# Optimization experiments

Hardware: AMD Instinct MI355X
Metric: run time of the kernel (lower is better)

## Reference

```python
import jax, jax.numpy as jnp
import numpy as np

NUM_NODES = 80000
NUM_EDGES = 1280000
NUM_GRAPHS = 512
IN_DIM = 64
HID = 64
NUM_CLASSES = 10


def setup_inputs() -> dict:
    key = jax.random.key(0)
    ks = jax.random.split(key, 16)
    x = jax.random.normal(ks[0], (NUM_NODES, IN_DIM), dtype=jnp.float32)
    edge_index = jax.random.randint(ks[1], (2, NUM_EDGES), 0, NUM_NODES, dtype=jnp.int64)
    batch = jnp.sort(jax.random.randint(ks[2], (NUM_NODES,), 0, NUM_GRAPHS, dtype=jnp.int64))

    def glorot(k, shape):
        fan_in, fan_out = shape[1], shape[0]
        lim = jnp.sqrt(6.0 / (fan_in + fan_out))
        return jax.random.uniform(k, shape, dtype=jnp.float32, minval=-lim, maxval=lim)

    inp = {
        "x": x,
        "edge_index": edge_index,
        "batch": batch,
        # GraphConv layer 1: lin_rel (with bias) applied to aggregated neighbors, lin_root (no bias)
        "w_rel1": glorot(ks[3], (HID, IN_DIM)),
        "b_rel1": jnp.zeros((HID,), dtype=jnp.float32),
        "w_root1": glorot(ks[4], (HID, IN_DIM)),
        # layer 2
        "w_rel2": glorot(ks[5], (HID, HID)),
        "b_rel2": jnp.zeros((HID,), dtype=jnp.float32),
        "w_root2": glorot(ks[6], (HID, HID)),
        # layer 3
        "w_rel3": glorot(ks[7], (HID, HID)),
        "b_rel3": jnp.zeros((HID,), dtype=jnp.float32),
        "w_root3": glorot(ks[8], (HID, HID)),
        # final linear head
        "w_lin": glorot(ks[9], (NUM_CLASSES, HID)),
        "b_lin": jnp.zeros((NUM_CLASSES,), dtype=jnp.float32),
    }
    return inp


def _graph_conv(x, src, dst, w_rel, b_rel, w_root):
    # PyG GraphConv with aggr='add': out_i = W_rel @ (sum_{j in N(i)} x_j) + b_rel + W_root @ x_i
    agg = jax.ops.segment_sum(x[src], dst, num_segments=NUM_NODES)  # [N, d_in]
    return agg @ w_rel.T + b_rel + x @ w_root.T


def reference(x, edge_index, batch,
              w_rel1, b_rel1, w_root1,
              w_rel2, b_rel2, w_root2,
              w_rel3, b_rel3, w_root3,
              w_lin, b_lin):
    src, dst = edge_index[0], edge_index[1]
    h = jax.nn.relu(_graph_conv(x, src, dst, w_rel1, b_rel1, w_root1))
    h = jax.nn.relu(_graph_conv(h, src, dst, w_rel2, b_rel2, w_root2))
    h = _graph_conv(h, src, dst, w_rel3, b_rel3, w_root3)
    # global_mean_pool over graph ids
    sums = jax.ops.segment_sum(h, batch, num_segments=NUM_GRAPHS)          # [G, HID]
    counts = jax.ops.segment_sum(jnp.ones((h.shape[0],), h.dtype), batch, num_segments=NUM_GRAPHS)
    pooled = sums / jnp.maximum(counts, 1.0)[:, None]
    # dropout p=0.5 is identity at inference (training=False)
    return pooled @ w_lin.T + b_lin  # [G, NUM_CLASSES]
```

## Files before the change

kernel.cpp:

```cpp
#include <hip/hip_runtime.h>

#define N_NODES  80000
#define N_EDGES  1280000
#define N_GRAPHS 512
#define DIM      64
#define NCLS     10

#define ETILE    8192
#define NTILE    157
#define NCB      157
#define CBPAD    160

typedef short short8f __attribute__((ext_vector_type(8)));
typedef float float4f __attribute__((ext_vector_type(4)));

static __device__ __forceinline__ unsigned short f2bf(float f) {
    unsigned u = __float_as_uint(f);
    unsigned r = (u + 0x7FFFu + ((u >> 16) & 1u)) >> 16;
    return (unsigned short)r;
}
static __device__ __forceinline__ float bf_lo(unsigned v) { return __uint_as_float(v << 16); }
static __device__ __forceinline__ float bf_hi(unsigned v) { return __uint_as_float(v & 0xFFFF0000u); }

__global__ __launch_bounds__(256) void k_histprep(const int* __restrict__ ei,
        const float* __restrict__ x,
        const float* __restrict__ wr1, const float* __restrict__ wo1,
        const float* __restrict__ wr2, const float* __restrict__ wo2,
        int* __restrict__ hmat, unsigned short* __restrict__ xb,
        unsigned short* __restrict__ wf) {
    __shared__ int hist[NCB];
    int bid = blockIdx.x, t = threadIdx.x;
    if (bid < NTILE) {
        int tile = bid;
        for (int i = t; i < NCB; i += 256) hist[i] = 0;
        __syncthreads();
        int base = tile * ETILE;
        int end = base + ETILE; if (end > N_EDGES) end = N_EDGES;
        for (int i = base + t; i < end; i += 256)
            atomicAdd(&hist[ei[N_EDGES + i] >> 9], 1);
        __syncthreads();
        for (int i = t; i < NCB; i += 256) hmat[tile * CBPAD + i] = hist[i];
        return;
    }
    int pb = bid - NTILE;
    if (pb < 5000) {
        int i = pb * 256 + t;
        float4 v = ((const float4*)x)[i];
        ushort4 o;
        o.x = f2bf(v.x); o.y = f2bf(v.y); o.z = f2bf(v.z); o.w = f2bf(v.w);
        ((ushort4*)xb)[i] = o;
    } else {
        int idx = (pb - 5000) * 256 + t;
        int j = idx & 7, lane = (idx >> 3) & 63;
        int ks = (idx >> 9) & 3, nt = (idx >> 11) & 3, l = idx >> 13;
        int k = ks * 32 + ((lane >> 4) & 3) * 8 + j;
        int n = nt * 16 + (lane & 15);
        const float* wr = (l == 0) ? wr1 : wr2;
        const float* wo = (l == 0) ? wo1 : wo2;
        float val = (k < 64) ? wr[n * 64 + k] : wo[n * 64 + (k - 64)];
        wf[idx] = f2bf(val);
    }
}

__global__ __launch_bounds__(256) void k_scanT(const int* __restrict__ hmat,
        int* __restrict__ obase, int* __restrict__ btot) {
    __shared__ int sa[256], sb[256];
    int b = blockIdx.x, t = threadIdx.x;
    int v = (t < NTILE) ? hmat[t * CBPAD + b] : 0;
    sa[t] = v; __syncthreads();
    int* sp = sa; int* dp = sb;
    for (int off = 1; off < 256; off <<= 1) {
        dp[t] = sp[t] + ((t >= off) ? sp[t - off] : 0);
        __syncthreads();
        int* tmp = sp; sp = dp; dp = tmp;
    }
    int incl = sp[t];
    if (t < NTILE) obase[t * CBPAD + b] = incl - v;
    if (t == NTILE - 1) btot[b] = incl;
}

__global__ __launch_bounds__(256) void k_scatter2(const int* __restrict__ ei,
        const int* __restrict__ obase, const int* __restrict__ btot,
        int* __restrict__ ebuf) {
    __shared__ int sa[256], sb[256];
    __shared__ int cur[NCB];
    int tile = blockIdx.x, t = threadIdx.x;
    int v = (t < NCB) ? btot[t] : 0;
    sa[t] = v; __syncthreads();
    int* sp = sa; int* dp = sb;
    for (int off = 1; off < 256; off <<= 1) {
        dp[t] = sp[t] + ((t >= off) ? sp[t - off] : 0);
        __syncthreads();
        int* tmp = sp; sp = dp; dp = tmp;
    }
    if (t < NCB) cur[t] = (sp[t] - v) + obase[tile * CBPAD + t];
    __syncthreads();
    int base = tile * ETILE;
    int end = base + ETILE; if (end > N_EDGES) end = N_EDGES;
    for (int i = base + t; i < end; i += 256) {
        int s = ei[i], d = ei[N_EDGES + i];
        int p = atomicAdd(&cur[d >> 9], 1);
        ebuf[p] = s | ((d & 511) << 17);
    }
}

__global__ __launch_bounds__(256) void k_csr2(const int* __restrict__ ebuf,
        const int* __restrict__ btot, int* __restrict__ rowptr,
        int* __restrict__ col) {
    __shared__ int cnt[512];
    __shared__ int sa[512], sb[512];
    __shared__ int cur[512];
    int b = blockIdx.x, t = threadIdx.x;
    int v = (t < NCB) ? btot[t] : 0;
    sa[t] = v; __syncthreads();
    int* sp = sa; int* dp = sb;
    for (int off = 1; off < 256; off <<= 1) {
        dp[t] = sp[t] + ((t >= off) ? sp[t - off] : 0);
        __syncthreads();
        int* tmp = sp; sp = dp; dp = tmp;
    }
    int e = sp[b];
    int s = e - btot[b];
    if (b == 0 && t == 0) rowptr[N_NODES] = N_EDGES;
    __syncthreads();
    cnt[t] = 0; cnt[t + 256] = 0;
    __syncthreads();
    for (int i = s + t; i < e; i += 256) atomicAdd(&cnt[ebuf[i] >> 17], 1);
    __syncthreads();
    sa[t] = cnt[t]; sa[t + 256] = cnt[t + 256];
    __syncthreads();
    sp = sa; dp = sb;
    for (int off = 1; off < 512; off <<= 1) {
        int i1 = t + 256;
        int v0 = sp[t]  + ((t  >= off) ? sp[t  - off] : 0);
        int v1 = sp[i1] + ((i1 >= off) ? sp[i1 - off] : 0);
        __syncthreads();
        dp[t] = v0; dp[i1] = v1;
        __syncthreads();
        int* tmp = sp; sp = dp; dp = tmp;
    }
    int node0 = b * 512;
    int base0 = s + sp[t] - cnt[t];
    int base1 = s + sp[t + 256] - cnt[t + 256];
    cur[t] = base0; cur[t + 256] = base1;
    if (node0 + t < N_NODES)       rowptr[node0 + t] = base0;
    if (node0 + t + 256 < N_NODES) rowptr[node0 + t + 256] = base1;
    __syncthreads();
    for (int i = s + t; i < e; i += 256) {
        int pk = ebuf[i];
        int p = atomicAdd(&cur[pk >> 17], 1);
        col[p] = pk & 0x1FFFF;
    }
}

__global__ __launch_bounds__(256) void k_gatherlin(
        const unsigned short* __restrict__ Xin,
        const int* __restrict__ rowptr, const int* __restrict__ col,
        const unsigned short* __restrict__ wf, const float* __restrict__ bias,
        unsigned short* __restrict__ out, int relu) {
    __shared__ uint4 sAgg[64][9];
    const uint4* Xq = (const uint4*)Xin;
    int t = threadIdx.x, w = t >> 6, lane = t & 63;
    int e = lane >> 3, c = lane & 7;
    int nb = blockIdx.x * 64 + w * 16;
    int rp = (lane <= 16) ? rowptr[nb + lane] : 0;
    for (int n = 0; n < 16; ++n) {
        int start = __shfl(rp, n), end = __shfl(rp, n + 1);
        float acc[8] = {0.f, 0.f, 0.f, 0.f, 0.f, 0.f, 0.f, 0.f};
        int base = start;
        for (; base + 16 <= end; base += 16) {
            int i0 = col[base + e];
            int i1 = col[base + 8 + e];
            uint4 v0 = Xq[(size_t)i0 * 8 + c];
            uint4 v1 = Xq[(size_t)i1 * 8 + c];
            acc[0] += bf_lo(v0.x) + bf_lo(v1.x); acc[1] += bf_hi(v0.x) + bf_hi(v1.x);
            acc[2] += bf_lo(v0.y) + bf_lo(v1.y); acc[3] += bf_hi(v0.y) + bf_hi(v1.y);
            acc[4] += bf_lo(v0.z) + bf_lo(v1.z); acc[5] += bf_hi(v0.z) + bf_hi(v1.z);
            acc[6] += bf_lo(v0.w) + bf_lo(v1.w); acc[7] += bf_hi(v0.w) + bf_hi(v1.w);
        }
        for (; base + 8 <= end; base += 8) {
            int i0 = col[base + e];
            uint4 v0 = Xq[(size_t)i0 * 8 + c];
            acc[0] += bf_lo(v0.x); acc[1] += bf_hi(v0.x);
            acc[2] += bf_lo(v0.y); acc[3] += bf_hi(v0.y);
            acc[4] += bf_lo(v0.z); acc[5] += bf_hi(v0.z);
            acc[6] += bf_lo(v0.w); acc[7] += bf_hi(v0.w);
        }
        int r = end - base;
        if (e < r) {
            int i0 = col[base + e];
            uint4 v0 = Xq[(size_t)i0 * 8 + c];
            acc[0] += bf_lo(v0.x); acc[1] += bf_hi(v0.x);
            acc[2] += bf_lo(v0.y); acc[3] += bf_hi(v0.y);
            acc[4] += bf_lo(v0.z); acc[5] += bf_hi(v0.z);
            acc[6] += bf_lo(v0.w); acc[7] += bf_hi(v0.w);
        }
#pragma unroll
        for (int off = 8; off < 64; off <<= 1) {
#pragma unroll
            for (int j = 0; j < 8; ++j) acc[j] += __shfl_xor(acc[j], off);
        }
        if (e == 0) {
            uint4 o;
            o.x = (unsigned)f2bf(acc[0]) | ((unsigned)f2bf(acc[1]) << 16);
            o.y = (unsigned)f2bf(acc[2]) | ((unsigned)f2bf(acc[3]) << 16);
            o.z = (unsigned)f2bf(acc[4]) | ((unsigned)f2bf(acc[5]) << 16);
            o.w = (unsigned)f2bf(acc[6]) | ((unsigned)f2bf(acc[7]) << 16);
            sAgg[w * 16 + n][c] = o;
        }
    }
    int quad = lane >> 4, l15 = lane & 15;
    int m = nb + l15;
    short8f a0 = *(const short8f*)&sAgg[w * 16 + l15][quad];
    short8f a1 = *(const short8f*)&sAgg[w * 16 + l15][4 + quad];
    const unsigned short* xr = Xin + (size_t)m * 64;
    short8f a2 = *(const short8f*)(xr + quad * 8);
    short8f a3 = *(const short8f*)(xr + 32 + quad * 8);
    int orow = nb + quad * 4;
#pragma unroll
    for (int nt = 0; nt < 4; ++nt) {
        const unsigned short* wp = wf + ((size_t)(nt * 4) * 64 + lane) * 8;
        short8f b0 = *(const short8f*)(wp);
        short8f b1 = *(const short8f*)(wp + 64 * 8);
        short8f b2 = *(const short8f*)(wp + 128 * 8);
        short8f b3 = *(const short8f*)(wp + 192 * 8);
        float4f acc = {0.f, 0.f, 0.f, 0.f};
        acc = __builtin_amdgcn_mfma_f32_16x16x32_bf16(a0, b0, acc, 0, 0, 0);
        acc = __builtin_amdgcn_mfma_f32_16x16x32_bf16(a1, b1, acc, 0, 0, 0);
        acc = __builtin_amdgcn_mfma_f32_16x16x32_bf16(a2, b2, acc, 0, 0, 0);
        acc = __builtin_amdgcn_mfma_f32_16x16x32_bf16(a3, b3, acc, 0, 0, 0);
        float bi = bias[nt * 16 + l15];
#pragma unroll
        for (int r = 0; r < 4; ++r) {
            float v = acc[r] + bi;
            if (relu) v = fmaxf(v, 0.f);
            out[(size_t)(orow + r) * 64 + nt * 16 + l15] = f2bf(v);
        }
    }
}

static __device__ __forceinline__ int lowerb(const int* a, int n, int key) {
    int lo = 0, hi = n;
    while (lo < hi) { int mid = (lo + hi) >> 1; if (a[mid] < key) lo = mid + 1; else hi = mid; }
    return lo;
}

__global__ __launch_bounds__(256) void k_gsum(const unsigned short* __restrict__ h2,
        const int* __restrict__ rowptr, const int* __restrict__ col,
        const int* __restrict__ batch, float* __restrict__ S4) {
    __shared__ float red1[8][64];
    __shared__ float red2[8][64];
    const unsigned* Xu = (const unsigned*)h2;
    int g = blockIdx.x >> 2, part = blockIdx.x & 3;
    int t = threadIdx.x;
    int hw = t >> 5, c = t & 31;
    int ns = lowerb(batch, N_NODES, g);
    int ne = lowerb(batch, N_NODES, g + 1);
    int a0 = ns + (int)(((long long)(ne - ns) * part) >> 2);
    int a1 = ns + (int)(((long long)(ne - ns) * (part + 1)) >> 2);
    int es = rowptr[a0], ee = rowptr[a1];
    float alo = 0.f, ahi = 0.f;
    int nfull = (ee - es) >> 7;
    int e0 = es + hw * 16;
    for (int b = 0; b < nfull; ++b, e0 += 128) {
        unsigned v[16];
#pragma unroll
        for (int j = 0; j < 16; ++j)
            v[j] = Xu[(size_t)col[e0 + j] * 32 + c];
#pragma unroll
        for (int j = 0; j < 16; ++j) { alo += bf_lo(v[j]); ahi += bf_hi(v[j]); }
    }
    for (int e = es + nfull * 128 + hw; e < ee; e += 8) {
        unsigned v = Xu[(size_t)col[e] * 32 + c];
        alo += bf_lo(v); ahi += bf_hi(v);
    }
    float blo = 0.f, bhi = 0.f;
    for (int i = a0 + hw; i < a1; i += 8) {
        unsigned v = Xu[(size_t)i * 32 + c];
        blo += bf_lo(v); bhi += bf_hi(v);
    }
    red1[hw][2 * c] = alo; red1[hw][2 * c + 1] = ahi;
    red2[hw][2 * c] = blo; red2[hw][2 * c + 1] = bhi;
    __syncthreads();
    if (t < 64) {
        float v = 0.f;
#pragma unroll
        for (int s = 0; s < 8; ++s) v += red1[s][t];
        S4[(size_t)blockIdx.x * 128 + t] = v;
    } else if (t < 128) {
        float v = 0.f;
#pragma unroll
        for (int s = 0; s < 8; ++s) v += red2[s][t - 64];
        S4[(size_t)blockIdx.x * 128 + 64 + (t - 64)] = v;
    }
}

__global__ __launch_bounds__(64) void k_head2(const float* __restrict__ S4,
        const int* __restrict__ batch,
        const float* __restrict__ wr3, const float* __restrict__ wo3,
        const float* __restrict__ b3,
        const float* __restrict__ wlin, const float* __restrict__ blin,
        float* __restrict__ out) {
    __shared__ float s1[64], s2[64], pl[64];
    int g = blockIdx.x, t = threadIdx.x;
    int ns = lowerb(batch, N_NODES, g);
    int ne = lowerb(batch, N_NODES, g + 1);
    float inv = 1.f / (float)((ne > ns) ? (ne - ns) : 1);
    const float* Sg = S4 + (size_t)g * 4 * 128;
    s1[t] = (Sg[t]       + Sg[128 + t]       + Sg[256 + t]       + Sg[384 + t]) * inv;
    s2[t] = (Sg[64 + t]  + Sg[192 + t]       + Sg[320 + t]       + Sg[448 + t]) * inv;
    __syncthreads();
    float acc = b3[t];
    for (int k = 0; k < 64; ++k)
        acc += s1[k] * wr3[t * 64 + k] + s2[k] * wo3[t * 64 + k];
    pl[t] = acc;
    __syncthreads();
    float myout = 0.f;
    for (int cls = 0; cls < NCLS; ++cls) {
        float vv = pl[t] * wlin[cls * 64 + t];
        for (int off = 32; off > 0; off >>= 1) vv += __shfl_xor(vv, off);
        if (t == cls) myout = vv + blin[cls];
    }
    if (t < NCLS) out[g * NCLS + t] = myout;
}

extern "C" void kernel_launch(void* const* d_in, const int* in_sizes, int n_in,
                              void* d_out, int out_size, void* d_ws, size_t ws_size,
                              hipStream_t stream) {
    const float* x     = (const float*)d_in[0];
    const int*   ei    = (const int*)d_in[1];
    const int*   batch = (const int*)d_in[2];
    const float* wr1 = (const float*)d_in[3];
    const float* b1  = (const float*)d_in[4];
    const float* wo1 = (const float*)d_in[5];
    const float* wr2 = (const float*)d_in[6];
    const float* b2  = (const float*)d_in[7];
    const float* wo2 = (const float*)d_in[8];
    const float* wr3 = (const float*)d_in[9];
    const float* b3  = (const float*)d_in[10];
    const float* wo3 = (const float*)d_in[11];
    const float* wlin = (const float*)d_in[12];
    const float* blin = (const float*)d_in[13];
    float* out = (float*)d_out;

    char* p = (char*)d_ws;
    auto alloc = [&](size_t bytes) { char* r = p; p += (bytes + 255) & ~(size_t)255; return r; };
    int*   rowptr  = (int*)alloc((N_NODES + 1) * sizeof(int));
    int*   hmat    = (int*)alloc((size_t)NTILE * CBPAD * sizeof(int));
    int*   obase   = (int*)alloc((size_t)NTILE * CBPAD * sizeof(int));
    int*   btot    = (int*)alloc(CBPAD * sizeof(int));
    int*   ebuf    = (int*)alloc((size_t)N_EDGES * sizeof(int));
    int*   col     = (int*)alloc((size_t)N_EDGES * sizeof(int));
    unsigned short* wf  = (unsigned short*)alloc(2 * 8192 * sizeof(unsigned short));
    unsigned short* xbf = (unsigned short*)alloc((size_t)N_NODES * 64 * 2);
    unsigned short* hA  = (unsigned short*)alloc((size_t)N_NODES * 64 * 2);
    unsigned short* hB  = (unsigned short*)alloc((size_t)N_NODES * 64 * 2);
    float* S4      = (float*)alloc((size_t)N_GRAPHS * 4 * 128 * sizeof(float));

    k_histprep<<<NTILE + 5064, 256, 0, stream>>>(ei, x, wr1, wo1, wr2, wo2,
                                                 hmat, xbf, wf);
    k_scanT   <<<NCB,   256, 0, stream>>>(hmat, obase, btot);
    k_scatter2<<<NTILE, 256, 0, stream>>>(ei, obase, btot, ebuf);
    k_csr2    <<<NCB,   256, 0, stream>>>(ebuf, btot, rowptr, col);

    k_gatherlin<<<N_NODES / 64, 256, 0, stream>>>(xbf, rowptr, col, wf,        b1, hA, 1);
    k_gatherlin<<<N_NODES / 64, 256, 0, stream>>>(hA,  rowptr, col, wf + 8192, b2, hB, 1);

    k_gsum <<<N_GRAPHS * 4, 256, 0, stream>>>(hB, rowptr, col, batch, S4);
    k_head2<<<N_GRAPHS,     64,  0, stream>>>(S4, batch, wr3, wo3, b3, wlin, blin, out);
}
```

Baseline: 261.7 us.

## Switch activations to fp16 with packed half accumulation and finer CSR bucketing

Stores node features and weights as fp16 instead of bf16, so neighbour aggregation accumulates in packed half8 vector adds and the cross-lane reduction shuffles packed halves, removing per-element unpack-to-float arithmetic. The MFMA calls switch to the f16 variant. Separately, the CSR build uses smaller edge tiles (2048) and 256-node destination buckets, giving more blocks for the histogram, scatter and per-bucket sort kernels, with the scans adapted to handle more entries per thread. Accumulating sums in fp16 lowers precision and risks overflow or accuracy loss on high-degree nodes.

New measurement: 238.7 us. -8.8%, faster.

```diff
diff --git a/kernel.cpp b/kernel.cpp
--- a/kernel.cpp
+++ b/kernel.cpp
@@ -6,21 +6,24 @@
 #define DIM      64
 #define NCLS     10
 
-#define ETILE    8192
-#define NTILE    157
-#define NCB      157
-#define CBPAD    160
-
-typedef short short8f __attribute__((ext_vector_type(8)));
+#define ETILE    2048
+#define NTILE    625
+#define NCB      313
+#define CBPAD    320
+
+typedef _Float16 half8f __attribute__((ext_vector_type(8)));
 typedef float float4f __attribute__((ext_vector_type(4)));
 
-static __device__ __forceinline__ unsigned short f2bf(float f) {
-    unsigned u = __float_as_uint(f);
-    unsigned r = (u + 0x7FFFu + ((u >> 16) & 1u)) >> 16;
-    return (unsigned short)r;
-}
-static __device__ __forceinline__ float bf_lo(unsigned v) { return __uint_as_float(v << 16); }
-static __device__ __forceinline__ float bf_hi(unsigned v) { return __uint_as_float(v & 0xFFFF0000u); }
+static __device__ __forceinline__ unsigned short f2h(float f) {
+    _Float16 h = (_Float16)f;
+    return __builtin_bit_cast(unsigned short, h);
+}
+static __device__ __forceinline__ float h_lo(unsigned v) {
+    return (float)__builtin_bit_cast(_Float16, (unsigned short)(v & 0xFFFF));
+}
+static __device__ __forceinline__ float h_hi(unsigned v) {
+    return (float)__builtin_bit_cast(_Float16, (unsigned short)(v >> 16));
+}
 
 __global__ __launch_bounds__(256) void k_histprep(const int* __restrict__ ei,
         const float* __restrict__ x,
@@ -35,9 +38,9 @@
         for (int i = t; i < NCB; i += 256) hist[i] = 0;
         __syncthreads();
         int base = tile * ETILE;
-        int end = base + ETILE; if (end > N_EDGES) end = N_EDGES;
+        int end = base + ETILE;
         for (int i = base + t; i < end; i += 256)
-            atomicAdd(&hist[ei[N_EDGES + i] >> 9], 1);
+            atomicAdd(&hist[ei[N_EDGES + i] >> 8], 1);
         __syncthreads();
         for (int i = t; i < NCB; i += 256) hmat[tile * CBPAD + i] = hist[i];
         return;
@@ -47,7 +50,7 @@
         int i = pb * 256 + t;
         float4 v = ((const float4*)x)[i];
         ushort4 o;
-        o.x = f2bf(v.x); o.y = f2bf(v.y); o.z = f2bf(v.z); o.w = f2bf(v.w);
+        o.x = f2h(v.x); o.y = f2h(v.y); o.z = f2h(v.z); o.w = f2h(v.w);
         ((ushort4*)xb)[i] = o;
     } else {
         int idx = (pb - 5000) * 256 + t;
@@ -58,7 +61,7 @@
         const float* wr = (l == 0) ? wr1 : wr2;
         const float* wo = (l == 0) ? wo1 : wo2;
         float val = (k < 64) ? wr[n * 64 + k] : wo[n * 64 + (k - 64)];
-        wf[idx] = f2bf(val);
+        wf[idx] = f2h(val);
     }
 }
 
@@ -66,85 +69,96 @@
         int* __restrict__ obase, int* __restrict__ btot) {
     __shared__ int sa[256], sb[256];
     int b = blockIdx.x, t = threadIdx.x;
-    int v = (t < NTILE) ? hmat[t * CBPAD + b] : 0;
-    sa[t] = v; __syncthreads();
+    int j0 = 3 * t;
+    int l0 = (j0     < NTILE) ? hmat[(j0    ) * CBPAD + b] : 0;
+    int l1 = (j0 + 1 < NTILE) ? hmat[(j0 + 1) * CBPAD + b] : 0;
+    int l2 = (j0 + 2 < NTILE) ? hmat[(j0 + 2) * CBPAD + b] : 0;
+    int s = l0 + l1 + l2;
+    sa[t] = s; __syncthreads();
     int* sp = sa; int* dp = sb;
     for (int off = 1; off < 256; off <<= 1) {
         dp[t] = sp[t] + ((t >= off) ? sp[t - off] : 0);
         __syncthreads();
         int* tmp = sp; sp = dp; dp = tmp;
     }
-    int incl = sp[t];
-    if (t < NTILE) obase[t * CBPAD + b] = incl - v;
-    if (t == NTILE - 1) btot[b] = incl;
+    int ex = sp[t] - s;
+    if (j0     < NTILE) obase[(j0    ) * CBPAD + b] = ex;
+    if (j0 + 1 < NTILE) obase[(j0 + 1) * CBPAD + b] = ex + l0;
+    if (j0 + 2 < NTILE) obase[(j0 + 2) * CBPAD + b] = ex + l0 + l1;
+    if (t == 255) btot[b] = sp[255];
 }
 
 __global__ __launch_bounds__(256) void k_scatter2(const int* __restrict__ ei,
         const int* __restrict__ obase, const int* __restrict__ btot,
         int* __restrict__ ebuf) {
     __shared__ int sa[256], sb[256];
+    __shared__ int bbase[NCB];
     __shared__ int cur[NCB];
     int tile = blockIdx.x, t = threadIdx.x;
-    int v = (t < NCB) ? btot[t] : 0;
-    sa[t] = v; __syncthreads();
+    int l0 = (2 * t     < NCB) ? btot[2 * t]     : 0;
+    int l1 = (2 * t + 1 < NCB) ? btot[2 * t + 1] : 0;
+    int s = l0 + l1;
+    sa[t] = s; __syncthreads();
     int* sp = sa; int* dp = sb;
     for (int off = 1; off < 256; off <<= 1) {
         dp[t] = sp[t] + ((t >= off) ? sp[t - off] : 0);
         __syncthreads();
         int* tmp = sp; sp = dp; dp = tmp;
     }
-    if (t < NCB) cur[t] = (sp[t] - v) + obase[tile * CBPAD + t];
+    int ex = sp[t] - s;
+    if (2 * t     < NCB) bbase[2 * t]     = ex;
+    if (2 * t + 1 < NCB) bbase[2 * t + 1] = ex + l0;
+    __syncthreads();
+    for (int i = t; i < NCB; i += 256)
+        cur[i] = bbase[i] + obase[tile * CBPAD + i];
     __syncthreads();
     int base = tile * ETILE;
-    int end = base + ETILE; if (end > N_EDGES) end = N_EDGES;
+    int end = base + ETILE;
     for (int i = base + t; i < end; i += 256) {
-        int s = ei[i], d = ei[N_EDGES + i];
-        int p = atomicAdd(&cur[d >> 9], 1);
-        ebuf[p] = s | ((d & 511) << 17);
+        int sv = ei[i], d = ei[N_EDGES + i];
+        int p = atomicAdd(&cur[d >> 8], 1);
+        ebuf[p] = sv | ((d & 255) << 17);
     }
 }
 
 __global__ __launch_bounds__(256) void k_csr2(const int* __restrict__ ebuf,
         const int* __restrict__ btot, int* __restrict__ rowptr,
         int* __restrict__ col) {
-    __shared__ int cnt[512];
-    __shared__ int sa[512], sb[512];
-    __shared__ int cur[512];
+    __shared__ int sa[256], sb[256];
+    __shared__ int bbase[NCB];
+    __shared__ int cnt[256], cur[256];
     int b = blockIdx.x, t = threadIdx.x;
-    int v = (t < NCB) ? btot[t] : 0;
-    sa[t] = v; __syncthreads();
+    int l0 = (2 * t     < NCB) ? btot[2 * t]     : 0;
+    int l1 = (2 * t + 1 < NCB) ? btot[2 * t + 1] : 0;
+    int sm = l0 + l1;
+    sa[t] = sm; __syncthreads();
     int* sp = sa; int* dp = sb;
     for (int off = 1; off < 256; off <<= 1) {
         dp[t] = sp[t] + ((t >= off) ? sp[t - off] : 0);
         __syncthreads();
         int* tmp = sp; sp = dp; dp = tmp;
     }
-    int e = sp[b];
-    int s = e - btot[b];
-    if (b == 0 && t == 0) rowptr[N_NODES] = N_EDGES;
-    __syncthreads();
-    cnt[t] = 0; cnt[t + 256] = 0;
-    __syncthreads();
+    int ex = sp[t] - sm;
+    if (2 * t     < NCB) bbase[2 * t]     = ex;
+    if (2 * t + 1 < NCB) bbase[2 * t + 1] = ex + l0;
+    cnt[t] = 0;
+    __syncthreads();
+    int s = bbase[b];
+    int e = s + btot[b];
     for (int i = s + t; i < e; i += 256) atomicAdd(&cnt[ebuf[i] >> 17], 1);
     __syncthreads();
-    sa[t] = cnt[t]; sa[t + 256] = cnt[t + 256];
-    __syncthreads();
+    int c = cnt[t];
+    sa[t] = c; __syncthreads();
     sp = sa; dp = sb;
-    for (int off = 1; off < 512; off <<= 1) {
-        int i1 = t + 256;
-        int v0 = sp[t]  + ((t  >= off) ? sp[t  - off] : 0);
-        int v1 = sp[i1] + ((i1 >= off) ? sp[i1 - off] : 0);
-        __syncthreads();
-        dp[t] = v0; dp[i1] = v1;
+    for (int off = 1; off < 256; off <<= 1) {
+        dp[t] = sp[t] + ((t >= off) ? sp[t - off] : 0);
         __syncthreads();
         int* tmp = sp; sp = dp; dp = tmp;
     }
-    int node0 = b * 512;
-    int base0 = s + sp[t] - cnt[t];
-    int base1 = s + sp[t + 256] - cnt[t + 256];
-    cur[t] = base0; cur[t + 256] = base1;
-    if (node0 + t < N_NODES)       rowptr[node0 + t] = base0;
-    if (node0 + t + 256 < N_NODES) rowptr[node0 + t + 256] = base1;
+    int rowbase = s + sp[t] - c;
+    cur[t] = rowbase;
+    int node = b * 256 + t;
+    if (node <= N_NODES) rowptr[node] = rowbase;
     __syncthreads();
     for (int i = s + t; i < e; i += 256) {
         int pk = ebuf[i];
@@ -159,82 +173,68 @@
         const unsigned short* __restrict__ wf, const float* __restrict__ bias,
         unsigned short* __restrict__ out, int relu) {
     __shared__ uint4 sAgg[64][9];
-    const uint4* Xq = (const uint4*)Xin;
+    const half8f* Xq = (const half8f*)Xin;
     int t = threadIdx.x, w = t >> 6, lane = t & 63;
     int e = lane >> 3, c = lane & 7;
     int nb = blockIdx.x * 64 + w * 16;
     int rp = (lane <= 16) ? rowptr[nb + lane] : 0;
     for (int n = 0; n < 16; ++n) {
         int start = __shfl(rp, n), end = __shfl(rp, n + 1);
-        float acc[8] = {0.f, 0.f, 0.f, 0.f, 0.f, 0.f, 0.f, 0.f};
+        half8f acc = {};
         int base = start;
         for (; base + 16 <= end; base += 16) {
             int i0 = col[base + e];
             int i1 = col[base + 8 + e];
-            uint4 v0 = Xq[(size_t)i0 * 8 + c];
-            uint4 v1 = Xq[(size_t)i1 * 8 + c];
-            acc[0] += bf_lo(v0.x) + bf_lo(v1.x); acc[1] += bf_hi(v0.x) + bf_hi(v1.x);
-            acc[2] += bf_lo(v0.y) + bf_lo(v1.y); acc[3] += bf_hi(v0.y) + bf_hi(v1.y);
-            acc[4] += bf_lo(v0.z) + bf_lo(v1.z); acc[5] += bf_hi(v0.z) + bf_hi(v1.z);
-            acc[6] += bf_lo(v0.w) + bf_lo(v1.w); acc[7] += bf_hi(v0.w) + bf_hi(v1.w);
+            half8f v0 = Xq[(size_t)i0 * 8 + c];
+            half8f v1 = Xq[(size_t)i1 * 8 + c];
+            acc = acc + v0;
+            acc = acc + v1;
         }
         for (; base + 8 <= end; base += 8) {
             int i0 = col[base + e];
-            uint4 v0 = Xq[(size_t)i0 * 8 + c];
-            acc[0] += bf_lo(v0.x); acc[1] += bf_hi(v0.x);
-            acc[2] += bf_lo(v0.y); acc[3] += bf_hi(v0.y);
-            acc[4] += bf_lo(v0.z); acc[5] += bf_hi(v0.z);
-            acc[6] += bf_lo(v0.w); acc[7] += bf_hi(v0.w);
+            acc = acc + Xq[(size_t)i0 * 8 + c];
         }
         int r = end - base;
         if (e < r) {
             int i0 = col[base + e];
-            uint4 v0 = Xq[(size_t)i0 * 8 + c];
-            acc[0] += bf_lo(v0.x); acc[1] += bf_hi(v0.x);
-            acc[2] += bf_lo(v0.y); acc[3] += bf_hi(v0.y);
-            acc[4] += bf_lo(v0.z); acc[5] += bf_hi(v0.z);
-            acc[6] += bf_lo(v0.w); acc[7] += bf_hi(v0.w);
+            acc = acc + Xq[(size_t)i0 * 8 + c];
         }
 #pragma unroll
         for (int off = 8; off < 64; off <<= 1) {
-#pragma unroll
-            for (int j = 0; j < 8; ++j) acc[j] += __shfl_xor(acc[j], off);
-        }
-        if (e == 0) {
-            uint4 o;
-            o.x = (unsigned)f2bf(acc[0]) | ((unsigned)f2bf(acc[1]) << 16);
-            o.y = (unsigned)f2bf(acc[2]) | ((unsigned)f2bf(acc[3]) << 16);
-            o.z = (unsigned)f2bf(acc[4]) | ((unsigned)f2bf(acc[5]) << 16);
-            o.w = (unsigned)f2bf(acc[6]) | ((unsigned)f2bf(acc[7]) << 16);
-            sAgg[w * 16 + n][c] = o;
-        }
+            uint4 au = __builtin_bit_cast(uint4, acc);
+            uint4 bu;
+            bu.x = __shfl_xor(au.x, off); bu.y = __shfl_xor(au.y, off);
+            bu.z = __shfl_xor(au.z, off); bu.w = __shfl_xor(au.w, off);
+            acc = acc + __builtin_bit_cast(half8f, bu);
+        }
+        if (e == 0) sAgg[w * 16 + n][c] = __builtin_bit_cast(uint4, acc);
     }
     int quad = lane >> 4, l15 = lane & 15;
     int m = nb + l15;
-    short8f a0 = *(const short8f*)&sAgg[w * 16 + l15][quad];
-    short8f a1 = *(const short8f*)&sAgg[w * 16 + l15][4 + quad];
-    const unsigned short* xr = Xin + (size_t)m * 64;
-    short8f a2 = *(const short8f*)(xr + quad * 8);
-    short8f a3 = *(const short8f*)(xr + 32 + quad * 8);
+    half8f a0 = *(const half8f*)&sAgg[w * 16 + l15][quad];
+    half8f a1 = *(const half8f*)&sAgg[w * 16 + l15][4 + quad];
+    const half8f* xr = (const half8f*)(Xin + (size_t)m * 64);
+    half8f a2 = xr[quad];
+    half8f a3 = xr[4 + quad];
     int orow = nb + quad * 4;
 #pragma unroll
     for (int nt = 0; nt < 4; ++nt) {
-        const unsigned short* wp = wf + ((size_t)(nt * 4) * 64 + lane) * 8;
-        short8f b0 = *(const short8f*)(wp);
-        short8f b1 = *(const short8f*)(wp + 64 * 8);
-        short8f b2 = *(const short8f*)(wp + 128 * 8);
-        short8f b3 = *(const short8f*)(wp + 192 * 8);
+        const half8f* wp = (const half8f*)(wf + ((size_t)(nt * 4) * 64 + lane) * 8);
+        half8f b0 = wp[0];
+        half8f b1 = wp[64];
+        half8f b2 = wp[128];
+        half8f b3 = wp[192];
         float4f acc = {0.f, 0.f, 0.f, 0.f};
-        acc = __builtin_amdgcn_mfma_f32_16x16x32_bf16(a0, b0, acc, 0, 0, 0);
-        acc = __builtin_amdgcn_mfma_f32_16x16x32_bf16(a1, b1, acc, 0, 0, 0);
-        acc = __builtin_amdgcn_mfma_f32_16x16x32_bf16(a2, b2, acc, 0, 0, 0);
-        acc = __builtin_amdgcn_mfma_f32_16x16x32_bf16(a3, b3, acc, 0, 0, 0);
+        acc = __builtin_amdgcn_mfma_f32_16x16x32_f16(a0, b0, acc, 0, 0, 0);
+        acc = __builtin_amdgcn_mfma_f32_16x16x32_f16(a1, b1, acc, 0, 0, 0);
+        acc = __builtin_amdgcn_mfma_f32_16x16x32_f16(a2, b2, acc, 0, 0, 0);
+        acc = __builtin_amdgcn_mfma_f32_16x16x32_f16(a3, b3, acc, 0, 0, 0);
         float bi = bias[nt * 16 + l15];
 #pragma unroll
         for (int r = 0; r < 4; ++r) {
             float v = acc[r] + bi;
             if (relu) v = fmaxf(v, 0.f);
-            out[(size_t)(orow + r) * 64 + nt * 16 + l15] = f2bf(v);
+            out[(size_t)(orow + r) * 64 + nt * 16 + l15] = f2h(v);
         }
     }
 }
@@ -268,16 +268,16 @@
         for (int j = 0; j < 16; ++j)
             v[j] = Xu[(size_t)col[e0 + j] * 32 + c];
 #pragma unroll
-        for (int j = 0; j < 16; ++j) { alo += bf_lo(v[j]); ahi += bf_hi(v[j]); }
+        for (int j = 0; j < 16; ++j) { alo += h_lo(v[j]); ahi += h_hi(v[j]); }
     }
     for (int e = es + nfull * 128 + hw; e < ee; e += 8) {
         unsigned v = Xu[(size_t)col[e] * 32 + c];
-        alo += bf_lo(v); ahi += bf_hi(v);
+        alo += h_lo(v); ahi += h_hi(v);
     }
     float blo = 0.f, bhi = 0.f;
     for (int i = a0 + hw; i < a1; i += 8) {
         unsigned v = Xu[(size_t)i * 32 + c];
-        blo += bf_lo(v); bhi += bf_hi(v);
+        blo += h_lo(v); bhi += h_hi(v);
     }
     red1[hw][2 * c] = alo; red1[hw][2 * c + 1] = ahi;
     red2[hw][2 * c] = blo; red2[hw][2 * c + 1] = bhi;
```
